# Performance work log

Hardware: AMD Instinct MI355X
Metric: run time of the kernel (lower is better)

## Reference

```python
import jax, jax.numpy as jnp
import numpy as np

B, C, H, W = 4, 128, 64, 64


def setup_inputs() -> dict:
    key = jax.random.key(0)
    k1, k2 = jax.random.split(key)
    x = jax.random.normal(k1, (B, C, H, W), dtype=jnp.float32)
    # 1x1 conv kv_mapper: weight [C_out, C_in], bias [C_out]; C_out == C_in == C
    W_kv = jax.random.normal(k2, (C, C), dtype=jnp.float32) * (1.0 / np.sqrt(C))
    b_kv = jnp.zeros((C,), dtype=jnp.float32)
    return {"x": x, "W_kv": W_kv, "b_kv": b_kv}


def reference(x, W_kv, b_kv):
    b, c, h, w = x.shape
    # kv_mapper: 1x1 conv  -> v: [b, c, h, w]
    v = jnp.einsum('bchw,oc->bohw', x, W_kv) + b_kv[None, :, None, None]
    # rearrange 'b c h w -> b (h w) c'
    L = h * w
    values = v.reshape(b, c, L).transpose(0, 2, 1)    # keys == values
    queries = x.reshape(b, c, L).transpose(0, 2, 1)
    # scaled dot-product attention, full [b, L, L] scores
    scores = jnp.einsum('blc,btc->blt', queries, values) / jnp.sqrt(jnp.asarray(c, x.dtype))
    attn = jax.nn.softmax(scores, axis=-1)
    out = jnp.einsum('blt,btv->blv', attn, values)    # [b, L, c]
    # rearrange 'b (h w) c -> b c h w'
    return out.transpose(0, 2, 1).reshape(b, c, h, w)
```

## Files before the change

### kernel.cpp

```cpp
#include <hip/hip_runtime.h>

#define LQ 4096
#define CH 128
#define NB 4
#define QSCALE 0.12753139626233174f
#define ASTR 136
#define BSTR 72
#define MAXCH 8

#if defined(__has_builtin)
#if __has_builtin(__builtin_amdgcn_mfma_f32_16x16x16bf16_1k)
#define HAVE_MFMA16 1
#endif
#endif

typedef __attribute__((ext_vector_type(8))) unsigned short ushort8;
typedef __attribute__((ext_vector_type(4))) unsigned short ushort4v;
typedef __attribute__((ext_vector_type(4))) short short4v;
typedef __attribute__((ext_vector_type(8))) __bf16 bf16x8;
typedef __attribute__((ext_vector_type(4))) float f32x4;

__device__ inline unsigned short f2bf(float f) {
    unsigned int u = __builtin_bit_cast(unsigned int, f);
    u += 0x7fffu + ((u >> 16) & 1u);
    return (unsigned short)(u >> 16);
}
__device__ inline float bf2f(unsigned short h) {
    unsigned int u = (unsigned int)h << 16;
    return __builtin_bit_cast(float, u);
}
__device__ inline unsigned int bfpack2(float a, float b) {
    unsigned int ua = __builtin_bit_cast(unsigned int, a) + 0x8000u;
    unsigned int ub = __builtin_bit_cast(unsigned int, b) + 0x8000u;
    return (ua >> 16) | (ub & 0xffff0000u);
}

__global__ __launch_bounds__(256) void prep_kernel(
    const float* __restrict__ x, const float* __restrict__ Wkv,
    const float* __restrict__ bkv,
    unsigned short* __restrict__ Vt, unsigned short* __restrict__ Vc)
{
    __shared__ unsigned short vs[64 * 64];
    const int tid = threadIdx.x;
    const int lane = tid & 63;
    const int b = blockIdx.x & 3;
    const int l0 = ((blockIdx.x >> 2) & 63) << 6;
    const int ohalf = blockIdx.x >> 8;
    const int o0l = __builtin_amdgcn_readfirstlane((tid >> 6) << 4);

    float xr[CH];
    #pragma unroll
    for (int c = 0; c < CH; ++c)
        xr[c] = x[((size_t)b * CH + c) * LQ + l0 + lane];

    for (int oo = 0; oo < 16; oo += 2) {
        const int ol = o0l + oo;
        const int o = ohalf * 64 + ol;
        const float* wr0 = Wkv + (size_t)o * CH;
        const float* wr1 = wr0 + CH;
        float p0[4] = {bkv[o], 0.f, 0.f, 0.f};
        float p1[4] = {bkv[o + 1], 0.f, 0.f, 0.f};
        #pragma unroll
        for (int c = 0; c < CH; c += 4) {
            #pragma unroll
            for (int k = 0; k < 4; ++k) {
                p0[k] += wr0[c + k] * xr[c + k];
                p1[k] += wr1[c + k] * xr[c + k];
            }
        }
        const float a0 = (p0[0] + p0[1]) + (p0[2] + p0[3]);
        const float a1 = (p1[0] + p1[1]) + (p1[2] + p1[3]);
        const unsigned short h0 = f2bf(a0), h1 = f2bf(a1);
        Vc[((size_t)b * CH + o) * LQ + l0 + lane] = h0;
        Vc[((size_t)b * CH + o + 1) * LQ + l0 + lane] = h1;
        vs[ol * 64 + lane] = h0;
        vs[(ol + 1) * 64 + lane] = h1;
    }
    __syncthreads();
    #pragma unroll
    for (int i = 0; i < 2; ++i) {
        const int idx = i * 256 + tid;
        const int l = idx >> 3, og = idx & 7;
        ushort8 v;
        #pragma unroll
        for (int k = 0; k < 8; ++k) v[k] = vs[(og * 8 + k) * 64 + l];
        *(ushort8*)(Vt + ((size_t)b * LQ + l0 + l) * CH + ohalf * 64 + og * 8) = v;
    }
}

__global__ __launch_bounds__(256, 2) void attn_kernel(
    const float* __restrict__ x, const unsigned short* __restrict__ Vt,
    const unsigned short* __restrict__ Vc,
    unsigned short* __restrict__ Opart, float* __restrict__ Lsum, int titers)
{
    __shared__ __align__(16) unsigned short tileA[64 * ASTR];
    __shared__ __align__(16) unsigned short tileB[128 * BSTR];
    const int tid = threadIdx.x;
    const int wave = tid >> 6, lane = tid & 63;
    const int quad = lane >> 4, l16 = lane & 15;
    const int b = blockIdx.x & 3;
    const int rest = blockIdx.x >> 2;
    const int qtile = rest & 31;
    const int chunk = rest >> 5;
    const int q0w = (qtile << 7) + (wave << 5);
    const int tbase = chunk * titers * 64;

    const unsigned short* vtb = Vt + (size_t)b * LQ * CH;
    const unsigned short* vcb = Vc + (size_t)b * CH * LQ;

    bf16x8 qf[2][4];
    #pragma unroll
    for (int mt = 0; mt < 2; ++mt)
        #pragma unroll
        for (int kc = 0; kc < 4; ++kc) {
            ushort8 v;
            #pragma unroll
            for (int j = 0; j < 8; ++j) {
                int c = kc * 32 + quad * 8 + j;
                v[j] = f2bf(x[((size_t)b * CH + c) * LQ + q0w + mt * 16 + l16] * QSCALE);
            }
            qf[mt][kc] = __builtin_bit_cast(bf16x8, v);
        }

    f32x4 oacc[2][8];
    #pragma unroll
    for (int mt = 0; mt < 2; ++mt)
        #pragma unroll
        for (int i = 0; i < 8; ++i) oacc[mt][i] = f32x4{0.f, 0.f, 0.f, 0.f};
    float lsum[2] = {0.f, 0.f};

    ushort8 RA[4], RB[4];
    {
        const int t0 = tbase;
        #pragma unroll
        for (int i = 0; i < 4; ++i) {
            const int ci = i * 256 + tid;
            RA[i] = *(const ushort8*)(vtb + (size_t)(t0 + (ci >> 4)) * CH + (ci & 15) * 8);
        }
        #pragma unroll
        for (int i = 0; i < 4; ++i) {
            const int ci = i * 256 + tid;
            RB[i] = *(const ushort8*)(vcb + (size_t)(ci >> 3) * LQ + t0 + (ci & 7) * 8);
        }
    }

    for (int it = 0; it < titers; ++it) {
        __syncthreads();
        #pragma unroll
        for (int i = 0; i < 4; ++i) {
            const int ci = i * 256 + tid;
            *(ushort8*)(tileA + (ci >> 4) * ASTR + (ci & 15) * 8) = RA[i];
        }
        #pragma unroll
        for (int i = 0; i < 4; ++i) {
            const int ci = i * 256 + tid;
            *(ushort8*)(tileB + (ci >> 3) * BSTR + (ci & 7) * 8) = RB[i];
        }
        __syncthreads();
        {
            const int t0n = (it + 1 < titers) ? tbase + (it + 1) * 64 : tbase;
            #pragma unroll
            for (int i = 0; i < 4; ++i) {
                const int ci = i * 256 + tid;
                RA[i] = *(const ushort8*)(vtb + (size_t)(t0n + (ci >> 4)) * CH + (ci & 15) * 8);
            }
            #pragma unroll
            for (int i = 0; i < 4; ++i) {
                const int ci = i * 256 + tid;
                RB[i] = *(const ushort8*)(vcb + (size_t)(ci >> 3) * LQ + t0n + (ci & 7) * 8);
            }
        }
        #pragma unroll
        for (int nt = 0; nt < 4; ++nt) {
            bf16x8 vA[4];
            #pragma unroll
            for (int kc = 0; kc < 4; ++kc)
                vA[kc] = __builtin_bit_cast(bf16x8,
                    *(const ushort8*)(tileA + (nt * 16 + l16) * ASTR + kc * 32 + quad * 8));
            f32x4 s[2];
            #pragma unroll
            for (int mt = 0; mt < 2; ++mt) {
                s[mt] = f32x4{0.f, 0.f, 0.f, 0.f};
                #pragma unroll
                for (int kc = 0; kc < 4; ++kc)
                    s[mt] = __builtin_amdgcn_mfma_f32_16x16x32_bf16(vA[kc], qf[mt][kc], s[mt], 0, 0, 0);
            }
#ifdef HAVE_MFMA16
            short4v pf[2];
#else
            bf16x8 pf[2];
#endif
            #pragma unroll
            for (int mt = 0; mt < 2; ++mt) {
                float p0 = __builtin_amdgcn_exp2f(s[mt][0]);
                float p1 = __builtin_amdgcn_exp2f(s[mt][1]);
                float p2 = __builtin_amdgcn_exp2f(s[mt][2]);
                float p3 = __builtin_amdgcn_exp2f(s[mt][3]);
                lsum[mt] += (p0 + p1) + (p2 + p3);
                unsigned int lo = bfpack2(p0, p1);
                unsigned int hi = bfpack2(p2, p3);
#ifdef HAVE_MFMA16
                ushort4v pk;
                pk[0] = (unsigned short)lo; pk[1] = (unsigned short)(lo >> 16);
                pk[2] = (unsigned short)hi; pk[3] = (unsigned short)(hi >> 16);
                pf[mt] = __builtin_bit_cast(short4v, pk);
#else
                ushort8 pk;
                pk[0] = (unsigned short)lo; pk[1] = (unsigned short)(lo >> 16);
                pk[2] = (unsigned short)hi; pk[3] = (unsigned short)(hi >> 16);
                pk[4] = 0; pk[5] = 0; pk[6] = 0; pk[7] = 0;
                pf[mt] = __builtin_bit_cast(bf16x8, pk);
#endif
            }
            #pragma unroll
            for (int nc = 0; nc < 8; ++nc) {
                ushort4v d = *(const ushort4v*)(tileB +
                    (nc * 16 + l16) * BSTR + nt * 16 + quad * 4);
#ifdef HAVE_MFMA16
                short4v vB = __builtin_bit_cast(short4v, d);
                #pragma unroll
                for (int mt = 0; mt < 2; ++mt)
                    oacc[mt][nc] = __builtin_amdgcn_mfma_f32_16x16x16bf16_1k(
                        pf[mt], vB, oacc[mt][nc], 0, 0, 0);
#else
                ushort8 vb;
                vb[0] = d[0]; vb[1] = d[1]; vb[2] = d[2]; vb[3] = d[3];
                vb[4] = 0; vb[5] = 0; vb[6] = 0; vb[7] = 0;
                bf16x8 vB = __builtin_bit_cast(bf16x8, vb);
                #pragma unroll
                for (int mt = 0; mt < 2; ++mt)
                    oacc[mt][nc] = __builtin_amdgcn_mfma_f32_16x16x32_bf16(
                        pf[mt], vB, oacc[mt][nc], 0, 0, 0);
#endif
            }
        }
    }
    const size_t pbase = ((size_t)(chunk * NB + b) * LQ);
    #pragma unroll
    for (int mt = 0; mt < 2; ++mt) {
        float v = lsum[mt];
        v += __shfl_xor(v, 16);
        v += __shfl_xor(v, 32);
        if (lane < 16) Lsum[pbase + q0w + mt * 16 + lane] = v;
    }
    #pragma unroll
    for (int mt = 0; mt < 2; ++mt)
        #pragma unroll
        for (int r = 0; r < 4; ++r) {
            const int q = q0w + mt * 16 + quad * 4 + r;
            unsigned short* orow = Opart + (pbase + q) * CH + l16;
            #pragma unroll
            for (int nc = 0; nc < 8; ++nc) orow[nc * 16] = f2bf(oacc[mt][nc][r]);
        }
}

__global__ __launch_bounds__(256) void combine_kernel(
    const unsigned short* __restrict__ Opart, const float* __restrict__ Lsum,
    float* __restrict__ out, int nchunk)
{
    __shared__ __align__(16) float ls[32 * 132];
    __shared__ float linv[32];
    const int tid = threadIdx.x;
    const int b = blockIdx.x & 3;
    const int q0 = (blockIdx.x >> 2) << 5;

    if (tid < 32) {
        float s = 0.f;
        for (int ch = 0; ch < nchunk; ++ch) s += Lsum[(size_t)(ch * NB + b) * LQ + q0 + tid];
        linv[tid] = 1.0f / s;
    }
    __syncthreads();
    {
        const int c8 = (tid & 15) * 8, qg = tid >> 4;
        #pragma unroll
        for (int i = 0; i < 2; ++i) {
            const int q = qg * 2 + i;
            float s[8];
            #pragma unroll
            for (int k = 0; k < 8; ++k) s[k] = 0.f;
            for (int ch = 0; ch < nchunk; ++ch) {
                ushort8 p = *(const ushort8*)(Opart +
                    ((size_t)(ch * NB + b) * LQ + q0 + q) * CH + c8);
                #pragma unroll
                for (int k = 0; k < 8; ++k) s[k] += bf2f(p[k]);
            }
            const float li = linv[q];
            f32x4 o0, o1;
            #pragma unroll
            for (int k = 0; k < 4; ++k) { o0[k] = s[k] * li; o1[k] = s[k + 4] * li; }
            *(f32x4*)(ls + q * 132 + c8) = o0;
            *(f32x4*)(ls + q * 132 + c8 + 4) = o1;
        }
    }
    __syncthreads();
    {
        const int c = tid & 127, qh = tid >> 7;
        float* dst = out + ((size_t)b * CH + c) * LQ + q0 + qh * 16;
        #pragma unroll
        for (int i = 0; i < 4; ++i) {
            f32x4 o;
            #pragma unroll
            for (int r = 0; r < 4; ++r) o[r] = ls[(qh * 16 + i * 4 + r) * 132 + c];
            ((f32x4*)dst)[i] = o;
        }
    }
}

extern "C" void kernel_launch(void* const* d_in, const int* in_sizes, int n_in,
                              void* d_out, int out_size, void* d_ws, size_t ws_size,
                              hipStream_t stream) {
    const float* x   = (const float*)d_in[0];
    const float* Wkv = (const float*)d_in[1];
    const float* bkv = (const float*)d_in[2];
    float* out = (float*)d_out;

    const size_t vElems = (size_t)NB * LQ * CH;
    unsigned short* Vt = (unsigned short*)d_ws;
    unsigned short* Vc = Vt + vElems;
    float* Lsum = (float*)(Vc + vElems);
    unsigned short* Opart = (unsigned short*)(Lsum + (size_t)MAXCH * NB * LQ);

    int nchunk = 4;
    const size_t fixed = 2 * vElems * 2 + (size_t)MAXCH * NB * LQ * 4;
    while (nchunk > 1 && fixed + (size_t)nchunk * NB * LQ * CH * 2 > ws_size) nchunk >>= 1;
    const int titers = (LQ / 64) / nchunk;

    prep_kernel<<<dim3(512), dim3(256), 0, stream>>>(x, Wkv, bkv, Vt, Vc);
    attn_kernel<<<dim3(128 * nchunk), dim3(256), 0, stream>>>(x, Vt, Vc, Opart, Lsum, titers);
    combine_kernel<<<dim3(512), dim3(256), 0, stream>>>(Opart, Lsum, out, nchunk);
}
```

Baseline: 135.7 us.

## Compute 1x1 conv projection with bf16 MFMA and raise split-KV chunk count

The prep kernel now stages an x tile as bf16 in shared memory and computes the kv projection with 16x16x32 bf16 MFMA instead of scalar fp32 FMAs. Each block handles all 128 output channels, so the grid is halved, and Vc/Vt are written with vectorized stores from a shared tile. This rounds x and the weights to bf16 before the projection, which adds some error. Separately, the attention split-KV chunk count rises from 4 to MAXCH (8) when the workspace allows, doubling attention blocks at the cost of more partial outputs for the combine step.

New measurement: 131.4 us. 1.03x faster.

```diff
diff --git a/kernel.cpp b/kernel.cpp
--- a/kernel.cpp
+++ b/kernel.cpp
@@ -40,51 +40,83 @@
     const float* __restrict__ bkv,
     unsigned short* __restrict__ Vt, unsigned short* __restrict__ Vc)
 {
-    __shared__ unsigned short vs[64 * 64];
+    __shared__ __align__(16) unsigned short xs[64 * 136];
+    __shared__ __align__(16) unsigned short vs[128 * 72];
     const int tid = threadIdx.x;
     const int lane = tid & 63;
+    const int wave = tid >> 6;
+    const int quad = lane >> 4, l16 = lane & 15;
     const int b = blockIdx.x & 3;
-    const int l0 = ((blockIdx.x >> 2) & 63) << 6;
-    const int ohalf = blockIdx.x >> 8;
-    const int o0l = __builtin_amdgcn_readfirstlane((tid >> 6) << 4);
-
-    float xr[CH];
-    #pragma unroll
-    for (int c = 0; c < CH; ++c)
-        xr[c] = x[((size_t)b * CH + c) * LQ + l0 + lane];
-
-    for (int oo = 0; oo < 16; oo += 2) {
-        const int ol = o0l + oo;
-        const int o = ohalf * 64 + ol;
-        const float* wr0 = Wkv + (size_t)o * CH;
-        const float* wr1 = wr0 + CH;
-        float p0[4] = {bkv[o], 0.f, 0.f, 0.f};
-        float p1[4] = {bkv[o + 1], 0.f, 0.f, 0.f};
-        #pragma unroll
-        for (int c = 0; c < CH; c += 4) {
-            #pragma unroll
-            for (int k = 0; k < 4; ++k) {
-                p0[k] += wr0[c + k] * xr[c + k];
-                p1[k] += wr1[c + k] * xr[c + k];
-            }
-        }
-        const float a0 = (p0[0] + p0[1]) + (p0[2] + p0[3]);
-        const float a1 = (p1[0] + p1[1]) + (p1[2] + p1[3]);
-        const unsigned short h0 = f2bf(a0), h1 = f2bf(a1);
-        Vc[((size_t)b * CH + o) * LQ + l0 + lane] = h0;
-        Vc[((size_t)b * CH + o + 1) * LQ + l0 + lane] = h1;
-        vs[ol * 64 + lane] = h0;
-        vs[(ol + 1) * 64 + lane] = h1;
+    const int l0 = (blockIdx.x >> 2) << 6;
+
+    {
+        const f32x4* xg4 = (const f32x4*)(x + (size_t)b * CH * LQ + l0);
+        #pragma unroll
+        for (int i = 0; i < 8; ++i) {
+            int idx = i * 256 + tid;
+            int c = idx >> 4, l4 = idx & 15;
+            f32x4 v = xg4[c * (LQ / 4) + l4];
+            #pragma unroll
+            for (int m = 0; m < 4; ++m) xs[(l4 * 4 + m) * 136 + c] = f2bf(v[m]);
+        }
     }
     __syncthreads();
-    #pragma unroll
-    for (int i = 0; i < 2; ++i) {
-        const int idx = i * 256 + tid;
-        const int l = idx >> 3, og = idx & 7;
+
+    const int wo = wave * 32;
+    f32x4 acc[2][4];
+    #pragma unroll
+    for (int ot = 0; ot < 2; ++ot)
+        #pragma unroll
+        for (int lt = 0; lt < 4; ++lt) acc[ot][lt] = f32x4{0.f, 0.f, 0.f, 0.f};
+
+    #pragma unroll
+    for (int kc = 0; kc < 4; ++kc) {
+        bf16x8 af[2];
+        #pragma unroll
+        for (int ot = 0; ot < 2; ++ot) {
+            const float* wrow = Wkv + (size_t)(wo + ot * 16 + l16) * CH + kc * 32 + quad * 8;
+            ushort8 a;
+            #pragma unroll
+            for (int j = 0; j < 8; ++j) a[j] = f2bf(wrow[j]);
+            af[ot] = __builtin_bit_cast(bf16x8, a);
+        }
+        #pragma unroll
+        for (int lt = 0; lt < 4; ++lt) {
+            bf16x8 bf = __builtin_bit_cast(bf16x8,
+                *(const ushort8*)(xs + (lt * 16 + l16) * 136 + kc * 32 + quad * 8));
+            #pragma unroll
+            for (int ot = 0; ot < 2; ++ot)
+                acc[ot][lt] = __builtin_amdgcn_mfma_f32_16x16x32_bf16(af[ot], bf, acc[ot][lt], 0, 0, 0);
+        }
+    }
+    #pragma unroll
+    for (int ot = 0; ot < 2; ++ot) {
+        float bias[4];
+        #pragma unroll
+        for (int r = 0; r < 4; ++r) bias[r] = bkv[wo + ot * 16 + quad * 4 + r];
+        #pragma unroll
+        for (int lt = 0; lt < 4; ++lt)
+            #pragma unroll
+            for (int r = 0; r < 4; ++r)
+                vs[(wo + ot * 16 + quad * 4 + r) * 72 + lt * 16 + l16] =
+                    f2bf(acc[ot][lt][r] + bias[r]);
+    }
+    __syncthreads();
+    #pragma unroll
+    for (int i = 0; i < 4; ++i) {
+        const int chunk = i * 256 + tid;
+        const int o = chunk >> 3, l8 = chunk & 7;
+        *(ushort8*)(Vc + ((size_t)b * CH + o) * LQ + l0 + l8 * 8) =
+            *(const ushort8*)(vs + o * 72 + l8 * 8);
+    }
+    #pragma unroll
+    for (int i = 0; i < 4; ++i) {
+        const int chunk = i * 256 + tid;
+        const int l = chunk >> 4, og = chunk & 15;
         ushort8 v;
         #pragma unroll
-        for (int k = 0; k < 8; ++k) v[k] = vs[(og * 8 + k) * 64 + l];
-        *(ushort8*)(Vt + ((size_t)b * LQ + l0 + l) * CH + ohalf * 64 + og * 8) = v;
+        for (int k = 0; k < 8; ++k) v[k] = vs[(og * 8 + k) * 72 + l];
+        *(ushort8*)(Vt + ((size_t)b * LQ + l0 + l) * CH + og * 8) = v;
     }
 }
 
@@ -320,12 +352,12 @@
     float* Lsum = (float*)(Vc + vElems);
     unsigned short* Opart = (unsigned short*)(Lsum + (size_t)MAXCH * NB * LQ);
 
-    int nchunk = 4;
+    int nchunk = MAXCH;
     const size_t fixed = 2 * vElems * 2 + (size_t)MAXCH * NB * LQ * 4;
     while (nchunk > 1 && fixed + (size_t)nchunk * NB * LQ * CH * 2 > ws_size) nchunk >>= 1;
     const int titers = (LQ / 64) / nchunk;
 
-    prep_kernel<<<dim3(512), dim3(256), 0, stream>>>(x, Wkv, bkv, Vt, Vc);
+    prep_kernel<<<dim3(256), dim3(256), 0, stream>>>(x, Wkv, bkv, Vt, Vc);
     attn_kernel<<<dim3(128 * nchunk), dim3(256), 0, stream>>>(x, Vt, Vc, Opart, Lsum, titers);
     combine_kernel<<<dim3(512), dim3(256), 0, stream>>>(Opart, Lsum, out, nchunk);
 }
```
